# Kernel tuning notes

Hardware: AMD Instinct MI355X
Metric: run time of the kernel (lower is better)

The kernel has to match this reference:

```python
import jax, jax.numpy as jnp
import numpy as np

N_USERS = 100000
N_ITEMS = 200000
N_NODES = N_USERS + N_ITEMS
LATENT_DIM = 64
N_LAYERS = 3
NNZ = 6400000


def setup_inputs() -> dict:
    key = jax.random.key(0)
    k1, k2, k3, k4, k5 = jax.random.split(key, 5)
    user_emb = 0.1 * jax.random.normal(k1, (N_USERS, LATENT_DIM), dtype=jnp.float32)
    item_emb = 0.1 * jax.random.normal(k2, (N_ITEMS, LATENT_DIM), dtype=jnp.float32)
    rows = jax.random.randint(k3, (NNZ,), 0, N_NODES, dtype=jnp.int32)
    cols = jax.random.randint(k4, (NNZ,), 0, N_NODES, dtype=jnp.int32)
    # normalized-adjacency-like positive values
    vals = jax.random.uniform(k5, (NNZ,), dtype=jnp.float32) * 0.05
    return {"user_emb": user_emb, "item_emb": item_emb,
            "rows": rows, "cols": cols, "vals": vals}


def _spmm(rows, cols, vals, x):
    # y[r] += vals[e] * x[cols[e]]  for each edge e with rows[e]==r
    gathered = vals[:, None] * x[cols]          # [nnz, D]
    return jax.ops.segment_sum(gathered, rows, num_segments=N_NODES)


def reference(user_emb, item_emb, rows, cols, vals):
    # LightGCN.computer(): multi-hop propagation + layer mean pooling
    all_emb = jnp.concatenate([user_emb, item_emb], axis=0)   # [N, D]
    acc = all_emb
    for _ in range(N_LAYERS):
        all_emb = _spmm(rows, cols, vals, all_emb)
        acc = acc + all_emb
    light_out = acc / (N_LAYERS + 1)
    users = light_out[:N_USERS]
    items = light_out[N_USERS:]
    return users, items
```

## Files before the change

### kernel.cpp

```cpp
#include <hip/hip_runtime.h>
#include <hip/hip_bf16.h>

#define N_USERS 100000
#define N_ITEMS 200000
#define N_NODES 300000
#define DIM 64

#define TOT_ELEMS ((size_t)N_NODES * DIM)
#define TOT_F4    (TOT_ELEMS / 4)
#define USER_F4   (((size_t)N_USERS * DIM) / 4)

#define BROWS 512
#define NBUCKET ((N_NODES + BROWS - 1) / BROWS)
#define EPT 32
#define EDGES_PER_BLOCK (EPT * 256)

typedef float f4_native __attribute__((ext_vector_type(4)));

__device__ __forceinline__ float bf2f(unsigned short u) {
    return __uint_as_float((unsigned int)u << 16);
}
__device__ __forceinline__ unsigned short f2bf(float f) {
    __hip_bfloat16 h = __float2bfloat16(f);
    return *reinterpret_cast<unsigned short*>(&h);
}
__device__ __forceinline__ float lo_bf(unsigned int u) {
    return __uint_as_float(u << 16);
}
__device__ __forceinline__ float hi_bf(unsigned int u) {
    return __uint_as_float(u & 0xFFFF0000u);
}

__global__ void init_kernel(const float* __restrict__ user,
                            const float* __restrict__ item,
                            ushort4* __restrict__ xh) {
    size_t i = (size_t)blockIdx.x * blockDim.x + threadIdx.x;
    if (i >= TOT_F4) return;
    f4_native v = (i < USER_F4)
        ? __builtin_nontemporal_load((const f4_native*)user + i)
        : __builtin_nontemporal_load((const f4_native*)item + (i - USER_F4));
    ushort4 h;
    h.x = f2bf(v.x); h.y = f2bf(v.y); h.z = f2bf(v.z); h.w = f2bf(v.w);
    xh[i] = h;
}

__global__ void zero_buckets_kernel(int* __restrict__ bucket_count) {
    int i = blockIdx.x * blockDim.x + threadIdx.x;
    if (i < NBUCKET) bucket_count[i] = 0;
}

__global__ void bucket_hist_kernel(const int* __restrict__ rows,
                                   int* __restrict__ bucket_count, int nnz) {
    __shared__ int h[NBUCKET];
    int t = threadIdx.x;
    size_t base = (size_t)blockIdx.x * EDGES_PER_BLOCK;
    for (int i = t; i < NBUCKET; i += 256) h[i] = 0;
    __syncthreads();
    #pragma unroll 4
    for (int k = 0; k < EPT; ++k) {
        size_t e = base + (size_t)k * 256 + t;
        if (e < (size_t)nnz) atomicAdd(&h[rows[e] >> 9], 1);
    }
    __syncthreads();
    for (int i = t; i < NBUCKET; i += 256) {
        int c = h[i];
        if (c) atomicAdd(&bucket_count[i], c);
    }
}

__global__ void bucket_scan_kernel(const int* __restrict__ bucket_count,
                                   int* __restrict__ bucket_base,
                                   int* __restrict__ bucket_cursor, int nnz) {
    __shared__ int s[1024];
    int t = threadIdx.x;
    int orig = (t < NBUCKET) ? bucket_count[t] : 0;
    s[t] = orig;
    __syncthreads();
    for (int off = 1; off < 1024; off <<= 1) {
        int v = (t >= off) ? s[t - off] : 0;
        __syncthreads();
        s[t] += v;
        __syncthreads();
    }
    if (t < NBUCKET) {
        int excl = s[t] - orig;
        bucket_base[t]   = excl;
        bucket_cursor[t] = excl;
    }
    if (t == 0) bucket_base[NBUCKET] = nnz;
}

__global__ void binA_kernel(const int* __restrict__ rows,
                            const int* __restrict__ cols,
                            const float* __restrict__ vals,
                            int* __restrict__ bucket_cursor,
                            int2* __restrict__ binned,
                            int nnz) {
    __shared__ int h[NBUCKET];
    int t = threadIdx.x;
    size_t base = (size_t)blockIdx.x * EDGES_PER_BLOCK;
    for (int i = t; i < NBUCKET; i += 256) h[i] = 0;
    __syncthreads();
    #pragma unroll 4
    for (int k = 0; k < EPT; ++k) {
        size_t e = base + (size_t)k * 256 + t;
        if (e < (size_t)nnz) atomicAdd(&h[rows[e] >> 9], 1);
    }
    __syncthreads();
    for (int i = t; i < NBUCKET; i += 256) {
        int c = h[i];
        h[i] = (c > 0) ? atomicAdd(&bucket_cursor[i], c) : 0;
    }
    __syncthreads();
    #pragma unroll 4
    for (int k = 0; k < EPT; ++k) {
        size_t e = base + (size_t)k * 256 + t;
        if (e < (size_t)nnz) {
            int r = rows[e];
            int pos = atomicAdd(&h[r >> 9], 1);
            int c   = __builtin_nontemporal_load(cols + e);
            float v = __builtin_nontemporal_load(vals + e);
            binned[pos] = make_int2(((r & (BROWS - 1)) << 19) | c,
                                    __float_as_int(v));
        }
    }
}

__global__ void binB_kernel(const int* __restrict__ bucket_base,
                            const int2* __restrict__ binned,
                            int2* __restrict__ sorted,
                            int* __restrict__ row_ptr,
                            int nnz) {
    __shared__ int cnt[BROWS];
    __shared__ int cur[BROWS];
    __shared__ int s[256];
    int b = blockIdx.x, t = threadIdx.x;
    int beg = bucket_base[b];
    int end = bucket_base[b + 1];
    int row0 = b * BROWS;
    for (int i = t; i < BROWS; i += 256) cnt[i] = 0;
    __syncthreads();
    for (int idx = beg + t; idx < end; idx += 256) {
        int lr = ((unsigned)binned[idx].x) >> 19;
        atomicAdd(&cnt[lr], 1);
    }
    __syncthreads();
    int c0 = cnt[2 * t], c1 = cnt[2 * t + 1];
    int local = c0 + c1;
    s[t] = local;
    __syncthreads();
    for (int off = 1; off < 256; off <<= 1) {
        int v = (t >= off) ? s[t - off] : 0;
        __syncthreads();
        s[t] += v;
        __syncthreads();
    }
    int excl = beg + s[t] - local;
    int r0 = row0 + 2 * t;
    if (r0 < N_NODES)     row_ptr[r0]     = excl;
    if (r0 + 1 < N_NODES) row_ptr[r0 + 1] = excl + c0;
    cur[2 * t]     = excl;
    cur[2 * t + 1] = excl + c0;
    __syncthreads();
    for (int idx = beg + t; idx < end; idx += 256) {
        int2 e = binned[idx];
        int lr  = ((unsigned)e.x) >> 19;
        int col = e.x & 0x7FFFF;
        int pos = atomicAdd(&cur[lr], 1);
        sorted[pos] = make_int2(col, e.y);
    }
    if (b == 0 && t == 0) row_ptr[N_NODES] = nnz;
}

__device__ __forceinline__ void row_accum2(int beg, int end, int l,
                                           const int2* __restrict__ sorted,
                                           const unsigned short* __restrict__ srch,
                                           float& r0, float& r1) {
    const int h4 = (l >> 5) << 2;
    const unsigned int q = (unsigned)(l & 31);
    const unsigned int* __restrict__ srcd = (const unsigned int*)srch;
    float acc0 = 0.f, acc1 = 0.f;

    for (int base = beg; base < end; base += 64) {
        int rem = end - base;
        int cnt = rem > 64 ? 64 : rem;
        int c_l = 0, v_l = 0;
        if (base + l < end) {
            unsigned long long e = __builtin_nontemporal_load(
                (const unsigned long long*)sorted + base + l);
            c_l = (int)(unsigned int)(e & 0xFFFFFFFFull);
            v_l = (int)(unsigned int)(e >> 32);
        }
        int npairs = (cnt + 1) >> 1;
        int p = 0;
        for (; p + 8 <= npairs; p += 8) {
            int i0 = h4 + (p << 3);
            int c0 = __builtin_amdgcn_ds_bpermute(i0 +  0, c_l);
            int c1 = __builtin_amdgcn_ds_bpermute(i0 +  8, c_l);
            int c2 = __builtin_amdgcn_ds_bpermute(i0 + 16, c_l);
            int c3 = __builtin_amdgcn_ds_bpermute(i0 + 24, c_l);
            int c4 = __builtin_amdgcn_ds_bpermute(i0 + 32, c_l);
            int c5 = __builtin_amdgcn_ds_bpermute(i0 + 40, c_l);
            int c6 = __builtin_amdgcn_ds_bpermute(i0 + 48, c_l);
            int c7 = __builtin_amdgcn_ds_bpermute(i0 + 56, c_l);
            unsigned int u0 = srcd[((unsigned int)c0 << 5) | q];
            unsigned int u1 = srcd[((unsigned int)c1 << 5) | q];
            unsigned int u2 = srcd[((unsigned int)c2 << 5) | q];
            unsigned int u3 = srcd[((unsigned int)c3 << 5) | q];
            unsigned int u4 = srcd[((unsigned int)c4 << 5) | q];
            unsigned int u5 = srcd[((unsigned int)c5 << 5) | q];
            unsigned int u6 = srcd[((unsigned int)c6 << 5) | q];
            unsigned int u7 = srcd[((unsigned int)c7 << 5) | q];
            float v0 = __int_as_float(__builtin_amdgcn_ds_bpermute(i0 +  0, v_l));
            float v1 = __int_as_float(__builtin_amdgcn_ds_bpermute(i0 +  8, v_l));
            float v2 = __int_as_float(__builtin_amdgcn_ds_bpermute(i0 + 16, v_l));
            float v3 = __int_as_float(__builtin_amdgcn_ds_bpermute(i0 + 24, v_l));
            float v4 = __int_as_float(__builtin_amdgcn_ds_bpermute(i0 + 32, v_l));
            float v5 = __int_as_float(__builtin_amdgcn_ds_bpermute(i0 + 40, v_l));
            float v6 = __int_as_float(__builtin_amdgcn_ds_bpermute(i0 + 48, v_l));
            float v7 = __int_as_float(__builtin_amdgcn_ds_bpermute(i0 + 56, v_l));
            acc0 = fmaf(v0, lo_bf(u0), acc0); acc1 = fmaf(v0, hi_bf(u0), acc1);
            acc0 = fmaf(v1, lo_bf(u1), acc0); acc1 = fmaf(v1, hi_bf(u1), acc1);
            acc0 = fmaf(v2, lo_bf(u2), acc0); acc1 = fmaf(v2, hi_bf(u2), acc1);
            acc0 = fmaf(v3, lo_bf(u3), acc0); acc1 = fmaf(v3, hi_bf(u3), acc1);
            acc0 = fmaf(v4, lo_bf(u4), acc0); acc1 = fmaf(v4, hi_bf(u4), acc1);
            acc0 = fmaf(v5, lo_bf(u5), acc0); acc1 = fmaf(v5, hi_bf(u5), acc1);
            acc0 = fmaf(v6, lo_bf(u6), acc0); acc1 = fmaf(v6, hi_bf(u6), acc1);
            acc0 = fmaf(v7, lo_bf(u7), acc0); acc1 = fmaf(v7, hi_bf(u7), acc1);
        }
        for (; p + 4 <= npairs; p += 4) {
            int i0 = h4 + (p << 3);
            int c0 = __builtin_amdgcn_ds_bpermute(i0 +  0, c_l);
            int c1 = __builtin_amdgcn_ds_bpermute(i0 +  8, c_l);
            int c2 = __builtin_amdgcn_ds_bpermute(i0 + 16, c_l);
            int c3 = __builtin_amdgcn_ds_bpermute(i0 + 24, c_l);
            unsigned int u0 = srcd[((unsigned int)c0 << 5) | q];
            unsigned int u1 = srcd[((unsigned int)c1 << 5) | q];
            unsigned int u2 = srcd[((unsigned int)c2 << 5) | q];
            unsigned int u3 = srcd[((unsigned int)c3 << 5) | q];
            float v0 = __int_as_float(__builtin_amdgcn_ds_bpermute(i0 +  0, v_l));
            float v1 = __int_as_float(__builtin_amdgcn_ds_bpermute(i0 +  8, v_l));
            float v2 = __int_as_float(__builtin_amdgcn_ds_bpermute(i0 + 16, v_l));
            float v3 = __int_as_float(__builtin_amdgcn_ds_bpermute(i0 + 24, v_l));
            acc0 = fmaf(v0, lo_bf(u0), acc0); acc1 = fmaf(v0, hi_bf(u0), acc1);
            acc0 = fmaf(v1, lo_bf(u1), acc0); acc1 = fmaf(v1, hi_bf(u1), acc1);
            acc0 = fmaf(v2, lo_bf(u2), acc0); acc1 = fmaf(v2, hi_bf(u2), acc1);
            acc0 = fmaf(v3, lo_bf(u3), acc0); acc1 = fmaf(v3, hi_bf(u3), acc1);
        }
        for (; p < npairs; ++p) {
            int i0 = h4 + (p << 3);
            int c0 = __builtin_amdgcn_ds_bpermute(i0, c_l);
            unsigned int u0 = srcd[((unsigned int)c0 << 5) | q];
            float v0 = __int_as_float(__builtin_amdgcn_ds_bpermute(i0, v_l));
            acc0 = fmaf(v0, lo_bf(u0), acc0);
            acc1 = fmaf(v0, hi_bf(u0), acc1);
        }
    }
    r0 = acc0 + __shfl_xor(acc0, 32);
    r1 = acc1 + __shfl_xor(acc1, 32);
}

__global__ void spmm_row_kernel(const int* __restrict__ row_ptr,
                                const int2* __restrict__ sorted,
                                const unsigned short* __restrict__ srch,
                                unsigned short* __restrict__ dsth) {
    int t = blockIdx.x * blockDim.x + threadIdx.x;
    int r = t >> 6;
    int l = t & 63;
    if (r >= N_NODES) return;
    float r0, r1;
    row_accum2(row_ptr[r], row_ptr[r + 1], l, sorted, srch, r0, r1);
    if (l < 32) {
        unsigned int pack = (unsigned int)f2bf(r0) | ((unsigned int)f2bf(r1) << 16);
        ((unsigned int*)dsth)[(size_t)r * 32 + l] = pack;
    }
}

__global__ void spmm_final_kernel(const int* __restrict__ row_ptr,
                                  const int2* __restrict__ sorted,
                                  const unsigned short* __restrict__ y2h,
                                  const unsigned short* __restrict__ y1h,
                                  const float* __restrict__ user,
                                  const float* __restrict__ item,
                                  float* __restrict__ out) {
    int t = blockIdx.x * blockDim.x + threadIdx.x;
    int r = t >> 6;
    int l = t & 63;
    if (r >= N_NODES) return;
    float r0, r1;
    row_accum2(row_ptr[r], row_ptr[r + 1], l, sorted, y2h, r0, r1);
    if (l < 32) {
        size_t didx = (size_t)r * 32 + l;
        unsigned int y1d = __builtin_nontemporal_load((const unsigned int*)y1h + didx);
        unsigned int y2d = __builtin_nontemporal_load((const unsigned int*)y2h + didx);
        const float* bp = (r < N_USERS) ? (user + 2 * didx)
                                        : (item + 2 * (didx - (size_t)N_USERS * 32));
        float b0 = __builtin_nontemporal_load(bp + 0);
        float b1 = __builtin_nontemporal_load(bp + 1);
        float o0 = 0.25f * (b0 + lo_bf(y1d) + lo_bf(y2d) + r0);
        float o1 = 0.25f * (b1 + hi_bf(y1d) + hi_bf(y2d) + r1);
        __builtin_nontemporal_store(o0, out + 2 * didx + 0);
        __builtin_nontemporal_store(o1, out + 2 * didx + 1);
    }
}

extern "C" void kernel_launch(void* const* d_in, const int* in_sizes, int n_in,
                              void* d_out, int out_size, void* d_ws, size_t ws_size,
                              hipStream_t stream) {
    const float* user = (const float*)d_in[0];
    const float* item = (const float*)d_in[1];
    const int*   rows = (const int*)d_in[2];
    const int*   cols = (const int*)d_in[3];
    const float* vals = (const float*)d_in[4];
    int nnz = in_sizes[2];

    float* out = (float*)d_out;

    char* p = (char*)d_ws;
    unsigned short* xh  = (unsigned short*)p; p += TOT_ELEMS * 2;
    unsigned short* y1h = (unsigned short*)p; p += TOT_ELEMS * 2;
    unsigned short* y2h = (unsigned short*)p; p += TOT_ELEMS * 2;
    int2* binned = (int2*)p; p += (size_t)nnz * sizeof(int2);
    int2* sorted = (int2*)p; p += (size_t)nnz * sizeof(int2);
    int* row_ptr       = (int*)p; p += (size_t)(N_NODES + 1) * 4;
    int* bucket_count  = (int*)p; p += (size_t)NBUCKET * 4;
    int* bucket_base   = (int*)p; p += (size_t)(NBUCKET + 1) * 4;
    int* bucket_cursor = (int*)p; p += (size_t)NBUCKET * 4;

    const int BLK = 256;
    int grid_elem = (int)((TOT_F4 + BLK - 1) / BLK);
    int grid_binA = (nnz + EDGES_PER_BLOCK - 1) / EDGES_PER_BLOCK;
    int grid_rows = (N_NODES * 64 + BLK - 1) / BLK;

    init_kernel<<<grid_elem, BLK, 0, stream>>>(user, item, (ushort4*)xh);

    zero_buckets_kernel<<<(NBUCKET + BLK - 1) / BLK, BLK, 0, stream>>>(bucket_count);
    bucket_hist_kernel<<<grid_binA, BLK, 0, stream>>>(rows, bucket_count, nnz);
    bucket_scan_kernel<<<1, 1024, 0, stream>>>(bucket_count, bucket_base, bucket_cursor, nnz);

    binA_kernel<<<grid_binA, BLK, 0, stream>>>(rows, cols, vals, bucket_cursor, binned, nnz);
    binB_kernel<<<NBUCKET, BLK, 0, stream>>>(bucket_base, binned, sorted, row_ptr, nnz);

    spmm_row_kernel<<<grid_rows, BLK, 0, stream>>>(row_ptr, sorted, xh,  y1h);
    spmm_row_kernel<<<grid_rows, BLK, 0, stream>>>(row_ptr, sorted, y1h, y2h);
    spmm_final_kernel<<<grid_rows, BLK, 0, stream>>>(row_ptr, sorted, y2h, y1h,
                                                     user, item, out);
}
```

Baseline: 887.8 us.

## Stage binned edges in shared memory before writing them out to global buckets

```diff
diff --git a/kernel.cpp b/kernel.cpp
--- a/kernel.cpp
+++ b/kernel.cpp
@@ -96,33 +96,74 @@
                             int* __restrict__ bucket_cursor,
                             int2* __restrict__ binned,
                             int nnz) {
-    __shared__ int h[NBUCKET];
+    __shared__ int  h[NBUCKET];
+    __shared__ int  lstart[NBUCKET];
+    __shared__ int  lcur[NBUCKET];
+    __shared__ int  gbase[NBUCKET];
+    __shared__ int  s[256];
+    __shared__ int2 ledge[EDGES_PER_BLOCK];
+
     int t = threadIdx.x;
     size_t base = (size_t)blockIdx.x * EDGES_PER_BLOCK;
+    int nvalid = (int)(((size_t)nnz - base < (size_t)EDGES_PER_BLOCK)
+                       ? ((size_t)nnz - base) : (size_t)EDGES_PER_BLOCK);
+
     for (int i = t; i < NBUCKET; i += 256) h[i] = 0;
     __syncthreads();
+
     #pragma unroll 4
     for (int k = 0; k < EPT; ++k) {
-        size_t e = base + (size_t)k * 256 + t;
-        if (e < (size_t)nnz) atomicAdd(&h[rows[e] >> 9], 1);
-    }
-    __syncthreads();
+        int e = k * 256 + t;
+        if (e < nvalid) atomicAdd(&h[rows[base + e] >> 9], 1);
+    }
+    __syncthreads();
+
+    int i0 = 3 * t, i1 = 3 * t + 1, i2 = 3 * t + 2;
+    int c0 = (i0 < NBUCKET) ? h[i0] : 0;
+    int c1 = (i1 < NBUCKET) ? h[i1] : 0;
+    int c2 = (i2 < NBUCKET) ? h[i2] : 0;
+    int g = c0 + c1 + c2;
+    s[t] = g;
+    __syncthreads();
+    for (int off = 1; off < 256; off <<= 1) {
+        int v = (t >= off) ? s[t - off] : 0;
+        __syncthreads();
+        s[t] += v;
+        __syncthreads();
+    }
+    int excl = s[t] - g;
+    if (i0 < NBUCKET) { lstart[i0] = excl;           lcur[i0] = excl; }
+    if (i1 < NBUCKET) { lstart[i1] = excl + c0;      lcur[i1] = excl + c0; }
+    if (i2 < NBUCKET) { lstart[i2] = excl + c0 + c1; lcur[i2] = excl + c0 + c1; }
+
     for (int i = t; i < NBUCKET; i += 256) {
         int c = h[i];
-        h[i] = (c > 0) ? atomicAdd(&bucket_cursor[i], c) : 0;
-    }
-    __syncthreads();
+        gbase[i] = c ? atomicAdd(&bucket_cursor[i], c) : 0;
+    }
+    __syncthreads();
+
     #pragma unroll 4
     for (int k = 0; k < EPT; ++k) {
-        size_t e = base + (size_t)k * 256 + t;
-        if (e < (size_t)nnz) {
-            int r = rows[e];
-            int pos = atomicAdd(&h[r >> 9], 1);
-            int c   = __builtin_nontemporal_load(cols + e);
-            float v = __builtin_nontemporal_load(vals + e);
-            binned[pos] = make_int2(((r & (BROWS - 1)) << 19) | c,
+        int e = k * 256 + t;
+        if (e < nvalid) {
+            size_t ge = base + e;
+            int r = rows[ge];
+            int c = __builtin_nontemporal_load(cols + ge);
+            float v = __builtin_nontemporal_load(vals + ge);
+            int slot = atomicAdd(&lcur[r >> 9], 1);
+            ledge[slot] = make_int2(((r & (BROWS - 1)) << 19) | c,
                                     __float_as_int(v));
         }
+    }
+    __syncthreads();
+
+    for (int slot = t; slot < nvalid; slot += 256) {
+        int lo = 0, hi = NBUCKET;
+        while (hi - lo > 1) {
+            int mid = (lo + hi) >> 1;
+            if (lstart[mid] <= slot) lo = mid; else hi = mid;
+        }
+        binned[gbase[lo] + (slot - lstart[lo])] = ledge[slot];
     }
 }
 
```

New measurement: 813.5 us. 8.4% less time.
